# Kernel optimization log

Hardware: AMD Instinct MI355X
Metric: run time of the kernel (lower is better)

Reference implementation:

```python
import jax, jax.numpy as jnp
import numpy as np

B, S, N = 16, 128, 64            # batch, sentence length, padded KB-word slots per sentence
E, DK, H, L = 128, 128, 128, 32  # char embed, kb embed, per-direction hidden (hidden_size=2H), labels
CHAR_NUM, KB_NUM = 8000, 200000


def setup_inputs():
    key = jax.random.key(0)
    ks = jax.random.split(key, 40)
    u = lambda k, sh: jax.random.uniform(k, sh, jnp.float32, -0.08, 0.08)
    inp = {
        "char_ids": jax.random.randint(ks[0], (B, S), 0, CHAR_NUM),
        "kb_word_ids": jax.random.randint(ks[1], (B, N), 0, KB_NUM),
        "word_begin": jax.random.randint(ks[2], (B, N), 0, S),
        "word_len": jax.random.randint(ks[3], (B, N), 0, 6),
        "label": jax.random.randint(ks[4], (B, S), 0, L),
        "sequence_length": jax.random.randint(ks[5], (B,), S // 2, S + 1),
        "char_emb": u(ks[6], (CHAR_NUM, E)),
        "kb_emb": u(ks[7], (KB_NUM, DK)),
        "dense_W": u(ks[8], (2 * H, L)),
        "dense_b": jnp.zeros((L,), jnp.float32),
        "crf_T": u(ks[9], (L, L)),
    }
    i = 10
    for p in ("f", "r"):
        inp[p + "_Wcx"] = u(ks[i], (E, 4 * H))
        inp[p + "_Wch"] = u(ks[i + 1], (H, 4 * H))
        inp[p + "_bc"] = jnp.zeros((4 * H,), jnp.float32)
        inp[p + "_Wwx"] = u(ks[i + 2], (DK, 3 * H))
        inp[p + "_Wwh"] = u(ks[i + 3], (H, 3 * H))
        inp[p + "_bw"] = jnp.zeros((3 * H,), jnp.float32)
        inp[p + "_Wlx"] = u(ks[i + 4], (E, H))
        inp[p + "_Wlc"] = u(ks[i + 5], (H, H))
        inp[p + "_bl"] = jnp.zeros((H,), jnp.float32)
        i += 6
    return inp


def _lattice_dir(X, Xw, begin, end, pos_valid, word_valid,
                 Wcx, Wch, bc, Wwx, Wwh, bw, Wlx, Wlc, bl):
    # X:[S,E] chars in scan order, Xw:[N,DK] KB words, begin/end:[N] span indices
    # in scan order (end inclusive), pos_valid:[S] bool, word_valid:[N] bool.
    Xg = X @ Wcx + bc    # [S,4H] hoisted char-gate input projection
    Xl = X @ Wlx + bl    # [S,H]  hoisted link-gate input projection
    Wg = Xw @ Wwx + bw   # [N,3H] hoisted word-gate input projection

    def step(carry, t):
        h_hist, c_hist = carry                 # [S+1,H]; slot k = state after step k-1
        h_prev, c_prev = h_hist[t], c_hist[t]
        gi, gf, go, gg = jnp.split(Xg[t] + h_prev @ Wch, 4)
        i = jax.nn.sigmoid(gi); f = jax.nn.sigmoid(gf)
        o = jax.nn.sigmoid(go); g = jnp.tanh(gg)
        # word cells: built from the state just before each word's begin position
        hb, cb = h_hist[begin], c_hist[begin]  # [N,H]
        wi, wf, wg = jnp.split(Wg + hb @ Wwh, 3, axis=1)
        cw = jax.nn.sigmoid(wf) * cb + jax.nn.sigmoid(wi) * jnp.tanh(wg)  # [N,H]
        lg = jax.nn.sigmoid(Xl[t] + cw @ Wlc)  # [N,H] link gates
        wmask = ((end == t) & word_valid).astype(X.dtype)[:, None]
        ew = jnp.exp(lg) * wmask
        ec = jnp.exp(i)
        c_lat = (ec * g + (ew * cw).sum(0)) / (ec + ew.sum(0))  # gate-normalized merge
        c_std = f * c_prev + i * g             # plain LSTM step when no word ends at t
        c_t = jnp.where(wmask.sum() > 0, c_lat, c_std)
        h_t = o * jnp.tanh(c_t)
        v = pos_valid[t]
        h_hist = h_hist.at[t + 1].set(jnp.where(v, h_t, h_prev))
        c_hist = c_hist.at[t + 1].set(jnp.where(v, c_t, c_prev))
        return (h_hist, c_hist), jnp.where(v, h_t, jnp.zeros_like(h_t))

    init = (jnp.zeros((S + 1, H), X.dtype), jnp.zeros((S + 1, H), X.dtype))
    _, hs = jax.lax.scan(step, init, jnp.arange(S))
    return hs  # [S,H]


def _forward(char_ids, kb_word_ids, word_begin, word_len, label, sequence_length,
             char_emb, kb_emb, dense_W, dense_b, crf_T, fparams, rparams):
    X = char_emb[char_ids]            # [B,S,E]
    Xw = kb_emb[kb_word_ids]          # [B,N,DK]
    end = jnp.minimum(word_begin + word_len, S - 1)   # inclusive span end
    word_valid = end < sequence_length[:, None]       # whole span inside sentence
    pos = jnp.arange(S)
    pv_f = pos[None, :] < sequence_length[:, None]
    fwd = jax.vmap(lambda x, xw, b, e, pv, wv:
                   _lattice_dir(x, xw, b, e, pv, wv, *fparams))(
        X, Xw, word_begin, end, pv_f, word_valid)
    # backward direction: flip time axis; span (b,e) maps to (S-1-e, S-1-b)
    pv_r = pos[None, :] >= (S - sequence_length)[:, None]
    bwd = jax.vmap(lambda x, xw, b, e, pv, wv:
                   _lattice_dir(x, xw, b, e, pv, wv, *rparams))(
        X[:, ::-1], Xw, S - 1 - end, S - 1 - word_begin, pv_r, word_valid)[:, ::-1]
    feats = jnp.concatenate([fwd, bwd], axis=-1)      # [B,S,2H]
    logits = feats @ dense_W + dense_b                # [B,S,L]
    # CRF negative log-likelihood
    mask = pv_f.astype(logits.dtype)                  # [B,S]
    emit = jnp.take_along_axis(logits, label[..., None], axis=2)[..., 0]
    trans = crf_T[label[:, :-1], label[:, 1:]]
    gold = (emit * mask).sum(1) + (trans * mask[:, 1:]).sum(1)

    def fstep(alpha, xs):
        logit_t, m_t = xs
        new = jax.scipy.special.logsumexp(alpha[:, :, None] + crf_T[None], axis=1) + logit_t
        return jnp.where(m_t[:, None] > 0, new, alpha), None

    alpha, _ = jax.lax.scan(fstep, logits[:, 0],
                            (logits[:, 1:].transpose(1, 0, 2), mask[:, 1:].T))
    logZ = jax.scipy.special.logsumexp(alpha, axis=1)
    return jnp.mean(logZ - gold)


def reference(char_ids, kb_word_ids, word_begin, word_len, label, sequence_length,
              char_emb, kb_emb, dense_W, dense_b, crf_T,
              f_Wcx, f_Wch, f_bc, f_Wwx, f_Wwh, f_bw, f_Wlx, f_Wlc, f_bl,
              r_Wcx, r_Wch, r_bc, r_Wwx, r_Wwh, r_bw, r_Wlx, r_Wlc, r_bl):
    fparams = (f_Wcx, f_Wch, f_bc, f_Wwx, f_Wwh, f_bw, f_Wlx, f_Wlc, f_bl)
    rparams = (r_Wcx, r_Wch, r_bc, r_Wwx, r_Wwh, r_bw, r_Wlx, r_Wlc, r_bl)
    return _forward(char_ids, kb_word_ids, word_begin, word_len, label, sequence_length,
                    char_emb, kb_emb, dense_W, dense_b, crf_T, fparams, rparams)
```

## Files before the change

kernel.cpp:

```cpp
#include <hip/hip_runtime.h>


typedef _Float16 f16x8 __attribute__((ext_vector_type(8)));
typedef float    f32x4 __attribute__((ext_vector_type(4)));

__device__ __forceinline__ float sigm(float x) { return 1.f / (1.f + __expf(-x)); }
__device__ __forceinline__ float tanh_fast(float x) {
    return 1.f - 2.f / (__expf(2.f * x) + 1.f);
}
__device__ __forceinline__ void bar_lgkm() {
    asm volatile("s_waitcnt lgkmcnt(0)\n\ts_barrier" ::: "memory");
}

__device__ __forceinline__ f32x4 mfma16(f16x8 a, f16x8 b, f32x4 c) {
    return __builtin_amdgcn_mfma_f32_16x16x32_f16(a, b, c, 0, 0, 0);
}

__global__ __launch_bounds__(256)
void gemm_char(const float* __restrict__ emb, const int* __restrict__ idx,
               const float* __restrict__ Wg0, const float* __restrict__ Wg1,
               const float* __restrict__ bg0, const float* __restrict__ bg1,
               const float* __restrict__ Wl0, const float* __restrict__ Wl1,
               const float* __restrict__ bl0, const float* __restrict__ bl1,
               float* __restrict__ outg, float* __restrict__ outl)
{
    constexpr int K = 128, RPB = 8, BLK = 256;
    const int y = blockIdx.y;
    const float* __restrict__ Wg = y ? Wg1 : Wg0;
    const float* __restrict__ bg = y ? bg1 : bg0;
    const float* __restrict__ Wl = y ? Wl1 : Wl0;
    const float* __restrict__ bl = y ? bl1 : bl0;
    float* __restrict__ og = outg + (size_t)y * 2048 * 512;
    float* __restrict__ ol = outl + (size_t)y * 2048 * 128;

    __shared__ __align__(16) float xs[RPB * K];
    __shared__ const float* srcs[RPB];
    const int tid = threadIdx.x;
    const int r0 = blockIdx.x * RPB;
    if (tid < RPB) {
        const int row = r0 + tid;
        const int bb = row >> 7, tt = row & 127;
        const int ts = y ? (127 - tt) : tt;
        srcs[tid] = emb + (size_t)idx[bb * 128 + ts] * K;
    }
    __syncthreads();
    constexpr int NQ = RPB * K / 4;
    for (int q = tid; q < NQ; q += BLK) {
        const int rr = q / (K / 4), qq = q - rr * (K / 4);
        ((float4*)xs)[q] = ((const float4*)srcs[rr])[qq];
    }
    __syncthreads();

    {
        constexpr int NJ4 = 128, RT = BLK / NJ4, RPT = RPB / RT;
        const int jq = tid % NJ4;
        const int rg = tid / NJ4;
        float4 acc[RPT];
#pragma unroll
        for (int r = 0; r < RPT; ++r) acc[r] = make_float4(0.f, 0.f, 0.f, 0.f);
        const float4* __restrict__ W4 = (const float4*)Wg;
#pragma unroll 4
        for (int k = 0; k < K; ++k) {
            const float4 wv = W4[(size_t)k * NJ4 + jq];
#pragma unroll
            for (int r = 0; r < RPT; ++r) {
                const float xv = xs[(rg * RPT + r) * K + k];
                acc[r].x = fmaf(xv, wv.x, acc[r].x);
                acc[r].y = fmaf(xv, wv.y, acc[r].y);
                acc[r].z = fmaf(xv, wv.z, acc[r].z);
                acc[r].w = fmaf(xv, wv.w, acc[r].w);
            }
        }
        const float4 bv = ((const float4*)bg)[jq];
#pragma unroll
        for (int r = 0; r < RPT; ++r) {
            const int row = r0 + rg * RPT + r;
            ((float4*)og)[(size_t)row * NJ4 + jq] =
                make_float4(acc[r].x + bv.x, acc[r].y + bv.y,
                            acc[r].z + bv.z, acc[r].w + bv.w);
        }
    }
    {
        constexpr int NJ4 = 32;
        const int jq = tid % NJ4;
        const int rg = tid / NJ4;
        float4 acc = make_float4(0.f, 0.f, 0.f, 0.f);
        const float4* __restrict__ W4 = (const float4*)Wl;
#pragma unroll 4
        for (int k = 0; k < K; ++k) {
            const float4 wv = W4[(size_t)k * NJ4 + jq];
            const float xv = xs[rg * K + k];
            acc.x = fmaf(xv, wv.x, acc.x);
            acc.y = fmaf(xv, wv.y, acc.y);
            acc.z = fmaf(xv, wv.z, acc.z);
            acc.w = fmaf(xv, wv.w, acc.w);
        }
        const float4 bv = ((const float4*)bl)[jq];
        const int row = r0 + rg;
        ((float4*)ol)[(size_t)row * NJ4 + jq] =
            make_float4(acc.x + bv.x, acc.y + bv.y, acc.z + bv.z, acc.w + bv.w);
    }
}

template <int K, int J, int RPB, int BLK>
__global__ __launch_bounds__(BLK)
void gemm_pair(const float* __restrict__ emb, const int* __restrict__ idx,
               const float* __restrict__ W0, const float* __restrict__ W1,
               const float* __restrict__ b0, const float* __restrict__ b1,
               float* __restrict__ out, int rowsTotal, int Sdim, int revmode)
{
    constexpr int NJ4 = J / 4;
    constexpr int RT  = BLK / NJ4;
    constexpr int RPT = RPB / RT;
    static_assert(BLK % NJ4 == 0 && RPB % RT == 0, "layout");
    const int y = blockIdx.y;
    const float* __restrict__ W    = y ? W1 : W0;
    const float* __restrict__ bias = y ? b1 : b0;
    float* __restrict__ outp = out + (size_t)y * rowsTotal * J;
    const int rev = (revmode && y) ? 1 : 0;

    __shared__ __align__(16) float xs[RPB * K];
    __shared__ const float* srcs[RPB];
    const int tid = threadIdx.x;
    const int r0 = blockIdx.x * RPB;
    if (tid < RPB) {
        const int row = r0 + tid;
        const float* s = nullptr;
        if (row < rowsTotal) {
            if (idx) {
                const int bb = row / Sdim, tt = row - bb * Sdim;
                const int ts = rev ? (Sdim - 1 - tt) : tt;
                s = emb + (size_t)idx[bb * Sdim + ts] * K;
            } else {
                s = emb + (size_t)row * K;
            }
        }
        srcs[tid] = s;
    }
    __syncthreads();
    constexpr int NQ = RPB * K / 4;
    for (int q = tid; q < NQ; q += BLK) {
        const int rr = q / (K / 4), qq = q - rr * (K / 4);
        const float4* s = (const float4*)srcs[rr];
        ((float4*)xs)[q] = s ? s[qq] : make_float4(0.f, 0.f, 0.f, 0.f);
    }
    __syncthreads();

    const int jq = tid % NJ4;
    const int rg = tid / NJ4;
    float4 acc[RPT];
#pragma unroll
    for (int r = 0; r < RPT; ++r) acc[r] = make_float4(0.f, 0.f, 0.f, 0.f);
    const float4* __restrict__ W4 = (const float4*)W;
#pragma unroll 4
    for (int k = 0; k < K; ++k) {
        const float4 wv = W4[(size_t)k * NJ4 + jq];
#pragma unroll
        for (int r = 0; r < RPT; ++r) {
            const float xv = xs[(rg * RPT + r) * K + k];
            acc[r].x = fmaf(xv, wv.x, acc[r].x);
            acc[r].y = fmaf(xv, wv.y, acc[r].y);
            acc[r].z = fmaf(xv, wv.z, acc[r].z);
            acc[r].w = fmaf(xv, wv.w, acc[r].w);
        }
    }
    const float4 bv = ((const float4*)bias)[jq];
#pragma unroll
    for (int r = 0; r < RPT; ++r) {
        const int row = r0 + rg * RPT + r;
        if (row < rowsTotal)
            ((float4*)outp)[(size_t)row * NJ4 + jq] =
                make_float4(acc[r].x + bv.x, acc[r].y + bv.y,
                            acc[r].z + bv.z, acc[r].w + bv.w);
    }
}

#define HH_BYTES (129 * 128 * 2)
#define CH_BYTES (129 * 128 * 4)
#define LAT_DYN_SMEM (HH_BYTES + CH_BYTES)

__global__ __launch_bounds__(512, 2)
void lattice_kernel(const float* __restrict__ Xg,
                    const float* __restrict__ Xl,
                    const float* __restrict__ Wgp,
                    const float* __restrict__ Wch_f, const float* __restrict__ Wch_r,
                    const float* __restrict__ Wwh_f, const float* __restrict__ Wwh_r,
                    const float* __restrict__ Wlc_f, const float* __restrict__ Wlc_r,
                    const int* __restrict__ word_begin, const int* __restrict__ word_len,
                    const int* __restrict__ seqlen,
                    float* __restrict__ feats)
{
    extern __shared__ __align__(16) char dyn_smem[];
    _Float16* hh = (_Float16*)dyn_smem;
    float*    ch = (float*)(dyn_smem + HH_BYTES);

    const int bdid = blockIdx.x;
    const int b = bdid >> 1, dir = bdid & 1;
    const int tid = threadIdx.x;
    const int wid = tid >> 6;
    const int ln  = tid & 63;
    const int lg  = ln >> 4;
    const int jm  = wid * 16 + (ln & 15);

    const float* Wch = dir ? Wch_r : Wch_f;
    const float* Wwh = dir ? Wwh_r : Wwh_f;
    const float* Wlc = dir ? Wlc_r : Wlc_f;

    f16x8 Bc[4][4];
#pragma unroll
    for (int g = 0; g < 4; ++g)
#pragma unroll
        for (int kt = 0; kt < 4; ++kt) {
            f16x8 v;
#pragma unroll
            for (int i = 0; i < 8; ++i)
                v[i] = (_Float16)Wch[(size_t)(kt * 32 + lg * 8 + i) * 512 + (g * 128 + jm)];
            Bc[g][kt] = v;
        }
    f16x8 Bw[3][4];
#pragma unroll
    for (int p = 0; p < 3; ++p)
#pragma unroll
        for (int kt = 0; kt < 4; ++kt) {
            f16x8 v;
#pragma unroll
            for (int i = 0; i < 8; ++i)
                v[i] = (_Float16)Wwh[(size_t)(kt * 32 + lg * 8 + i) * 384 + (p * 128 + jm)];
            Bw[p][kt] = v;
        }
    f16x8 Bl[4];
#pragma unroll
    for (int kt = 0; kt < 4; ++kt) {
        f16x8 v;
#pragma unroll
        for (int i = 0; i < 8; ++i)
            v[i] = (_Float16)Wlc[(size_t)(kt * 32 + lg * 8 + i) * 128 + jm];
        Bl[kt] = v;
    }

    __shared__ __align__(16) _Float16 cw2s[2][2][128];
    __shared__ int ev_start[129];
    __shared__ int cnts[128];
    __shared__ int fills[128];
    __shared__ short ev_word[64];
    __shared__ short wbeg_s[64];

    const int sl = seqlen[b];

    if (tid < 128) { cnts[tid] = 0; fills[tid] = 0; }
    __syncthreads();
    int myvalid = 0, myed = 0;
    if (tid < 64) {
        const int bg = word_begin[b * 64 + tid];
        const int lnw = word_len[b * 64 + tid];
        int ef = bg + lnw; if (ef > 127) ef = 127;
        myvalid = (ef < sl);
        const int bd_ = dir ? (127 - ef) : bg;
        const int ed_ = dir ? (127 - bg) : ef;
        wbeg_s[tid] = (short)bd_;
        myed = ed_;
        if (myvalid) atomicAdd(&cnts[ed_], 1);
    }
    __syncthreads();
    if (tid == 0) {
        int run = 0; ev_start[0] = 0;
        for (int t = 0; t < 128; ++t) { run += cnts[t]; ev_start[t + 1] = run; }
    }
    __syncthreads();
    if (tid < 64 && myvalid) {
        const int pos = atomicAdd(&fills[myed], 1);
        ev_word[ev_start[myed] + pos] = (short)tid;
    }
    if (tid < 128) { hh[tid] = (_Float16)0.f; ch[tid] = 0.f; }
    __syncthreads();

    const float* Xg_b = Xg + ((size_t)dir * 2048 + (size_t)b * 128) * 512;
    const float* Xl_b = Xl + ((size_t)dir * 2048 + (size_t)b * 128) * 128;
    const float* Wg_b = Wgp + ((size_t)dir * 1024 + (size_t)b * 64) * 384;

    float h_reg = 0.f, c_reg = 0.f;

    int   curE, cur_ec0;
    int   cur_bgs[2] = {0, 0};
    float cur_wgp[2][3] = {};
    float xg_cur[4];
    {
        curE = ev_start[1];
        cur_ec0 = curE < 2 ? curE : 2;
#pragma unroll
        for (int s = 0; s < 2; ++s)
            if (s < cur_ec0) {
                const int wd = __builtin_amdgcn_readfirstlane((int)ev_word[s]);
                cur_bgs[s] = __builtin_amdgcn_readfirstlane((int)wbeg_s[wd]);
                const float* wgr = Wg_b + (size_t)wd * 384;
                cur_wgp[s][0] = wgr[jm];
                cur_wgp[s][1] = wgr[128 + jm];
                cur_wgp[s][2] = wgr[256 + jm];
            }
#pragma unroll
        for (int g = 0; g < 4; ++g) xg_cur[g] = Xg_b[g * 128 + jm];
    }

    for (int t = 0; t < 128; ++t) {
        f16x8 A[4];
#pragma unroll
        for (int kt = 0; kt < 4; ++kt)
            A[kt] = ((const f16x8*)hh)[t * 16 + kt * 4 + lg];

        float xl = 0.f;
        if (curE > 0) xl = Xl_b[(size_t)t * 128 + jm];

        int   nxtE = 0, nxt_ec0 = 0;
        int   nxt_bgs[2] = {0, 0};
        float nxt_wgp[2][3] = {};
        float xg_nxt[4] = {0.f, 0.f, 0.f, 0.f};
        if (t < 127) {
            const int e0n = ev_start[t + 1];
            nxtE = ev_start[t + 2] - e0n;
            nxt_ec0 = nxtE < 2 ? nxtE : 2;
#pragma unroll
            for (int s = 0; s < 2; ++s)
                if (s < nxt_ec0) {
                    const int wd = __builtin_amdgcn_readfirstlane((int)ev_word[e0n + s]);
                    nxt_bgs[s] = __builtin_amdgcn_readfirstlane((int)wbeg_s[wd]);
                    const float* wgr = Wg_b + (size_t)wd * 384;
                    nxt_wgp[s][0] = wgr[jm];
                    nxt_wgp[s][1] = wgr[128 + jm];
                    nxt_wgp[s][2] = wgr[256 + jm];
                }
#pragma unroll
            for (int g = 0; g < 4; ++g)
                xg_nxt[g] = Xg_b[(size_t)(t + 1) * 512 + g * 128 + jm];
        }

        f32x4 d[4];
#pragma unroll
        for (int g = 0; g < 4; ++g) d[g] = (f32x4){0.f, 0.f, 0.f, 0.f};
#pragma unroll
        for (int kt = 0; kt < 4; ++kt)
#pragma unroll
            for (int g = 0; g < 4; ++g)
                d[g] = mfma16(A[kt], Bc[g][kt], d[g]);

        const float gi = sigm(d[0][0] + xg_cur[0]);
        const float gf = sigm(d[1][0] + xg_cur[1]);
        const float go = sigm(d[2][0] + xg_cur[2]);
        const float gg = tanh_fast(d[3][0] + xg_cur[3]);

        float accn = 0.f, accd = 0.f;
        if (curE > 0) {
            const int e0 = ev_start[t];
            float cwreg[2] = {0.f, 0.f};
#pragma unroll
            for (int s = 0; s < 2; ++s)
                if (s < cur_ec0) {
                    f16x8 Ab[4];
#pragma unroll
                    for (int kt = 0; kt < 4; ++kt)
                        Ab[kt] = ((const f16x8*)hh)[cur_bgs[s] * 16 + kt * 4 + lg];
                    f32x4 ep[3];
#pragma unroll
                    for (int p = 0; p < 3; ++p) ep[p] = (f32x4){0.f, 0.f, 0.f, 0.f};
#pragma unroll
                    for (int kt = 0; kt < 4; ++kt)
#pragma unroll
                        for (int p = 0; p < 3; ++p)
                            ep[p] = mfma16(Ab[kt], Bw[p][kt], ep[p]);
                    const float wi = cur_wgp[s][0] + ep[0][0];
                    const float wf = cur_wgp[s][1] + ep[1][0];
                    const float wv = cur_wgp[s][2] + ep[2][0];
                    const float cb = ch[(size_t)cur_bgs[s] * 128 + jm];
                    const float cwv = sigm(wf) * cb + sigm(wi) * tanh_fast(wv);
                    cwreg[s] = cwv;
                    if (ln < 16) cw2s[0][s][jm] = (_Float16)cwv;
                }
            bar_lgkm();
#pragma unroll
            for (int s = 0; s < 2; ++s)
                if (s < cur_ec0) {
                    f16x8 Ac[4];
#pragma unroll
                    for (int kt = 0; kt < 4; ++kt)
                        Ac[kt] = ((const f16x8*)(&cw2s[0][s][0]))[kt * 4 + lg];
                    f32x4 r = (f32x4){0.f, 0.f, 0.f, 0.f};
#pragma unroll
                    for (int kt = 0; kt < 4; ++kt)
                        r = mfma16(Ac[kt], Bl[kt], r);
                    const float lgv = sigm(xl + r[0]);
                    const float ew = __expf(lgv);
                    accn = fmaf(ew, cwreg[s], accn);
                    accd += ew;
                }
            for (int base2 = 2; base2 < curE; base2 += 2) {
                const int bb = (base2 >> 1) & 1;
                const int en = (curE - base2) < 2 ? (curE - base2) : 2;
                float cwr2[2] = {0.f, 0.f};
#pragma unroll
                for (int s = 0; s < 2; ++s)
                    if (s < en) {
                        const int wd = __builtin_amdgcn_readfirstlane((int)ev_word[e0 + base2 + s]);
                        const int bg2 = __builtin_amdgcn_readfirstlane((int)wbeg_s[wd]);
                        const float* wgr = Wg_b + (size_t)wd * 384;
                        const float wg0 = wgr[jm], wg1 = wgr[128 + jm], wg2 = wgr[256 + jm];
                        f16x8 Ab[4];
#pragma unroll
                        for (int kt = 0; kt < 4; ++kt)
                            Ab[kt] = ((const f16x8*)hh)[bg2 * 16 + kt * 4 + lg];
                        f32x4 ep[3];
#pragma unroll
                        for (int p = 0; p < 3; ++p) ep[p] = (f32x4){0.f, 0.f, 0.f, 0.f};
#pragma unroll
                        for (int kt = 0; kt < 4; ++kt)
#pragma unroll
                            for (int p = 0; p < 3; ++p)
                                ep[p] = mfma16(Ab[kt], Bw[p][kt], ep[p]);
                        const float wi = wg0 + ep[0][0];
                        const float wf = wg1 + ep[1][0];
                        const float wv = wg2 + ep[2][0];
                        const float cb = ch[(size_t)bg2 * 128 + jm];
                        const float cwv = sigm(wf) * cb + sigm(wi) * tanh_fast(wv);
                        cwr2[s] = cwv;
                        if (ln < 16) cw2s[bb][s][jm] = (_Float16)cwv;
                    }
                bar_lgkm();
#pragma unroll
                for (int s = 0; s < 2; ++s)
                    if (s < en) {
                        f16x8 Ac[4];
#pragma unroll
                        for (int kt = 0; kt < 4; ++kt)
                            Ac[kt] = ((const f16x8*)(&cw2s[bb][s][0]))[kt * 4 + lg];
                        f32x4 r = (f32x4){0.f, 0.f, 0.f, 0.f};
#pragma unroll
                        for (int kt = 0; kt < 4; ++kt)
                            r = mfma16(Ac[kt], Bl[kt], r);
                        const float lgv = sigm(xl + r[0]);
                        const float ew = __expf(lgv);
                        accn = fmaf(ew, cwr2[s], accn);
                        accd += ew;
                    }
            }
        }

        float c_t;
        if (curE > 0) {
            const float ec = __expf(gi);
            c_t = (ec * gg + accn) / (ec + accd);
        } else {
            c_t = gf * c_reg + gi * gg;
        }
        const float h_t = go * tanh_fast(c_t);
        const bool v = dir ? (t >= 128 - sl) : (t < sl);
        const float hn = v ? h_t : h_reg;
        const float cn = v ? c_t : c_reg;
        h_reg = hn; c_reg = cn;
        if (ln < 16) {
            hh[(size_t)(t + 1) * 128 + jm] = (_Float16)hn;
            ch[(size_t)(t + 1) * 128 + jm] = cn;
        }

        curE = nxtE; cur_ec0 = nxt_ec0;
        cur_bgs[0] = nxt_bgs[0]; cur_bgs[1] = nxt_bgs[1];
#pragma unroll
        for (int s = 0; s < 2; ++s) {
            cur_wgp[s][0] = nxt_wgp[s][0];
            cur_wgp[s][1] = nxt_wgp[s][1];
            cur_wgp[s][2] = nxt_wgp[s][2];
        }
#pragma unroll
        for (int g = 0; g < 4; ++g) xg_cur[g] = xg_nxt[g];
        bar_lgkm();
    }

    for (int i = tid; i < 128 * 128; i += 512) {
        const int t = i >> 7, j = i & 127;
        const bool v = dir ? (t >= 128 - sl) : (t < sl);
        const float hv = v ? (float)hh[(size_t)(t + 1) * 128 + j] : 0.f;
        const int s = dir ? (127 - t) : t;
        feats[((size_t)b * 128 + s) * 256 + dir * 128 + j] = hv;
    }
}

__global__ void crf_kernel(const float* __restrict__ logits,
                           const int* __restrict__ label,
                           const int* __restrict__ seqlen,
                           const float* __restrict__ T,
                           float* __restrict__ out_part)
{
    const int half = threadIdx.x >> 5;
    const int j    = threadIdx.x & 31;
    const int b    = blockIdx.x * 2 + half;

    float Tc[32];
#pragma unroll
    for (int i = 0; i < 32; ++i) Tc[i] = T[i * 32 + j];

    const float* lg = logits + (size_t)b * 128 * 32;
    const int* lab = label + b * 128;
    const int sl = seqlen[b];

    float g = 0.f;
#pragma unroll
    for (int r = 0; r < 4; ++r) {
        const int t = j + r * 32;
        if (t < sl) {
            g += lg[t * 32 + lab[t]];
            if (t >= 1) g += T[lab[t - 1] * 32 + lab[t]];
        }
    }
#pragma unroll
    for (int m = 16; m; m >>= 1) g += __shfl_xor(g, m, 32);

    __shared__ __align__(16) float alpha_s[2][32];
    float av = lg[j];
    alpha_s[half][j] = av;
    __syncthreads();
    for (int t = 1; t < 128; ++t) {
        float a[32];
        const float4* ap = (const float4*)alpha_s[half];
#pragma unroll
        for (int q = 0; q < 8; ++q) {
            const float4 v = ap[q];
            a[4 * q] = v.x; a[4 * q + 1] = v.y; a[4 * q + 2] = v.z; a[4 * q + 3] = v.w;
        }
        float m = -1e30f;
#pragma unroll
        for (int i = 0; i < 32; ++i) m = fmaxf(m, a[i] + Tc[i]);
        float s = 0.f;
#pragma unroll
        for (int i = 0; i < 32; ++i) s += __expf(a[i] + Tc[i] - m);
        float nv = m + __logf(s) + lg[t * 32 + j];
        if (t >= sl) nv = av;
        av = nv;
        __syncthreads();
        alpha_s[half][j] = av;
        __syncthreads();
    }
    float m2 = av;
#pragma unroll
    for (int m = 16; m; m >>= 1) m2 = fmaxf(m2, __shfl_xor(m2, m, 32));
    float s2 = __expf(av - m2);
#pragma unroll
    for (int m = 16; m; m >>= 1) s2 += __shfl_xor(s2, m, 32);
    if (j == 0) out_part[b] = (m2 + __logf(s2)) - g;
}

__global__ void finalize_kernel(const float* __restrict__ partb, float* __restrict__ out)
{
    if (threadIdx.x == 0 && blockIdx.x == 0) {
        float s = 0.f;
        for (int i = 0; i < 16; i++) s += partb[i];
        out[0] = s * (1.f / 16.f);
    }
}

extern "C" void kernel_launch(void* const* d_in, const int* in_sizes, int n_in,
                              void* d_out, int out_size, void* d_ws, size_t ws_size,
                              hipStream_t stream)
{
    (void)in_sizes; (void)n_in; (void)out_size; (void)ws_size;
    const int*   char_ids    = (const int*)d_in[0];
    const int*   kb_word_ids = (const int*)d_in[1];
    const int*   word_begin  = (const int*)d_in[2];
    const int*   word_len    = (const int*)d_in[3];
    const int*   label       = (const int*)d_in[4];
    const int*   seqlen      = (const int*)d_in[5];
    const float* char_emb    = (const float*)d_in[6];
    const float* kb_emb      = (const float*)d_in[7];
    const float* dense_W     = (const float*)d_in[8];
    const float* dense_b     = (const float*)d_in[9];
    const float* crf_T       = (const float*)d_in[10];
    const float* f_Wcx = (const float*)d_in[11];
    const float* f_Wch = (const float*)d_in[12];
    const float* f_bc  = (const float*)d_in[13];
    const float* f_Wwx = (const float*)d_in[14];
    const float* f_Wwh = (const float*)d_in[15];
    const float* f_bw  = (const float*)d_in[16];
    const float* f_Wlx = (const float*)d_in[17];
    const float* f_Wlc = (const float*)d_in[18];
    const float* f_bl  = (const float*)d_in[19];
    const float* r_Wcx = (const float*)d_in[20];
    const float* r_Wch = (const float*)d_in[21];
    const float* r_bc  = (const float*)d_in[22];
    const float* r_Wwx = (const float*)d_in[23];
    const float* r_Wwh = (const float*)d_in[24];
    const float* r_bw  = (const float*)d_in[25];
    const float* r_Wlx = (const float*)d_in[26];
    const float* r_Wlc = (const float*)d_in[27];
    const float* r_bl  = (const float*)d_in[28];

    float* ws = (float*)d_ws;
    size_t o = 0;
    float* Xg     = ws + o; o += (size_t)2 * 2048 * 512;
    float* Xl     = ws + o; o += (size_t)2 * 2048 * 128;
    float* Wg     = ws + o; o += (size_t)2 * 1024 * 384;
    float* feats  = ws + o; o += (size_t)2048 * 256;
    float* logits = ws + o; o += (size_t)2048 * 32;
    float* partb  = ws + o; o += 16;

    gemm_char<<<dim3(256, 2), 256, 0, stream>>>(
        char_emb, char_ids, f_Wcx, r_Wcx, f_bc, r_bc,
        f_Wlx, r_Wlx, f_bl, r_bl, Xg, Xl);
    gemm_pair<128, 384, 8, 192><<<dim3(128, 2), 192, 0, stream>>>(
        kb_emb, kb_word_ids, f_Wwx, r_Wwx, f_bw, r_bw, Wg, 1024, 64, 0);

    lattice_kernel<<<32, 512, LAT_DYN_SMEM, stream>>>(
        Xg, Xl, Wg, f_Wch, r_Wch, f_Wwh, r_Wwh, f_Wlc, r_Wlc,
        word_begin, word_len, seqlen, feats);

    gemm_pair<256, 32, 16, 128><<<dim3(128, 1), 128, 0, stream>>>(
        feats, nullptr, dense_W, dense_W, dense_b, dense_b, logits, 2048, 128, 0);
    crf_kernel<<<8, 64, 0, stream>>>(logits, label, seqlen, crf_T, partb);
    finalize_kernel<<<1, 64, 0, stream>>>(partb, (float*)d_out);
}
```

Measured before the change: 496.4 us.

## Fuse pre-GEMMs, dense projection into lattice, and finalize into CRF

Merges the char and KB-word input projections into a single launch, computes per-direction partial logits inside the lattice kernel with fp16 dot2 instead of writing feats and running a separate dense GEMM, and folds the final mean into the CRF kernel using an atomic completion counter. The goal is to cut three kernel launches and the round trip of the feats buffer through global memory. In exchange the dense projection now runs in fp16, which changes numerics, and correctness depends on the counter being reset by the pre-GEMM kernel on every call.

```diff
diff --git a/kernel.cpp b/kernel.cpp
--- a/kernel.cpp
+++ b/kernel.cpp
@@ -1,6 +1,7 @@
 #include <hip/hip_runtime.h>
 
 
+typedef _Float16 f16x2 __attribute__((ext_vector_type(2)));
 typedef _Float16 f16x8 __attribute__((ext_vector_type(8)));
 typedef float    f32x4 __attribute__((ext_vector_type(4)));
 
@@ -16,162 +17,158 @@
     return __builtin_amdgcn_mfma_f32_16x16x32_f16(a, b, c, 0, 0, 0);
 }
 
+#if defined(__has_builtin)
+#if __has_builtin(__builtin_amdgcn_fdot2)
+#define FDOT2(a, b, c) __builtin_amdgcn_fdot2((a), (b), (c), false)
+#endif
+#endif
+#ifndef FDOT2
+__device__ __forceinline__ float fdot2_sw(f16x2 a, f16x2 b, float c) {
+    return fmaf((float)a.x, (float)b.x, fmaf((float)a.y, (float)b.y, c));
+}
+#define FDOT2(a, b, c) fdot2_sw((a), (b), (c))
+#endif
+
 __global__ __launch_bounds__(256)
-void gemm_char(const float* __restrict__ emb, const int* __restrict__ idx,
-               const float* __restrict__ Wg0, const float* __restrict__ Wg1,
-               const float* __restrict__ bg0, const float* __restrict__ bg1,
-               const float* __restrict__ Wl0, const float* __restrict__ Wl1,
-               const float* __restrict__ bl0, const float* __restrict__ bl1,
-               float* __restrict__ outg, float* __restrict__ outl)
+void gemm_pre(const float* __restrict__ cemb, const int* __restrict__ cidx,
+              const float* __restrict__ kemb, const int* __restrict__ kidx,
+              const float* __restrict__ Wg0, const float* __restrict__ Wg1,
+              const float* __restrict__ bg0, const float* __restrict__ bg1,
+              const float* __restrict__ Wl0, const float* __restrict__ Wl1,
+              const float* __restrict__ bl0, const float* __restrict__ bl1,
+              const float* __restrict__ Ww0, const float* __restrict__ Ww1,
+              const float* __restrict__ bw0, const float* __restrict__ bw1,
+              float* __restrict__ outg, float* __restrict__ outl,
+              float* __restrict__ outw, int* __restrict__ done_cnt)
 {
     constexpr int K = 128, RPB = 8, BLK = 256;
     const int y = blockIdx.y;
-    const float* __restrict__ Wg = y ? Wg1 : Wg0;
-    const float* __restrict__ bg = y ? bg1 : bg0;
-    const float* __restrict__ Wl = y ? Wl1 : Wl0;
-    const float* __restrict__ bl = y ? bl1 : bl0;
-    float* __restrict__ og = outg + (size_t)y * 2048 * 512;
-    float* __restrict__ ol = outl + (size_t)y * 2048 * 128;
+    const int tid = threadIdx.x;
+    if (blockIdx.x == 0 && y == 0 && tid == 0) *done_cnt = 0;
 
     __shared__ __align__(16) float xs[RPB * K];
     __shared__ const float* srcs[RPB];
-    const int tid = threadIdx.x;
-    const int r0 = blockIdx.x * RPB;
-    if (tid < RPB) {
-        const int row = r0 + tid;
-        const int bb = row >> 7, tt = row & 127;
-        const int ts = y ? (127 - tt) : tt;
-        srcs[tid] = emb + (size_t)idx[bb * 128 + ts] * K;
-    }
-    __syncthreads();
-    constexpr int NQ = RPB * K / 4;
-    for (int q = tid; q < NQ; q += BLK) {
-        const int rr = q / (K / 4), qq = q - rr * (K / 4);
-        ((float4*)xs)[q] = ((const float4*)srcs[rr])[qq];
-    }
-    __syncthreads();
-
-    {
-        constexpr int NJ4 = 128, RT = BLK / NJ4, RPT = RPB / RT;
-        const int jq = tid % NJ4;
-        const int rg = tid / NJ4;
-        float4 acc[RPT];
-#pragma unroll
-        for (int r = 0; r < RPT; ++r) acc[r] = make_float4(0.f, 0.f, 0.f, 0.f);
-        const float4* __restrict__ W4 = (const float4*)Wg;
+
+    if (blockIdx.x < 256) {
+        const float* __restrict__ Wg = y ? Wg1 : Wg0;
+        const float* __restrict__ bg = y ? bg1 : bg0;
+        const float* __restrict__ Wl = y ? Wl1 : Wl0;
+        const float* __restrict__ bl = y ? bl1 : bl0;
+        float* __restrict__ og = outg + (size_t)y * 2048 * 512;
+        float* __restrict__ ol = outl + (size_t)y * 2048 * 128;
+
+        const int r0 = blockIdx.x * RPB;
+        if (tid < RPB) {
+            const int row = r0 + tid;
+            const int bb = row >> 7, tt = row & 127;
+            const int ts = y ? (127 - tt) : tt;
+            srcs[tid] = cemb + (size_t)cidx[bb * 128 + ts] * K;
+        }
+        __syncthreads();
+        constexpr int NQ = RPB * K / 4;
+        for (int q = tid; q < NQ; q += BLK) {
+            const int rr = q / (K / 4), qq = q - rr * (K / 4);
+            ((float4*)xs)[q] = ((const float4*)srcs[rr])[qq];
+        }
+        __syncthreads();
+
+        {
+            constexpr int NJ4 = 128, RT = BLK / NJ4, RPT = RPB / RT;
+            const int jq = tid % NJ4;
+            const int rg = tid / NJ4;
+            float4 acc[RPT];
+#pragma unroll
+            for (int r = 0; r < RPT; ++r) acc[r] = make_float4(0.f, 0.f, 0.f, 0.f);
+            const float4* __restrict__ W4 = (const float4*)Wg;
 #pragma unroll 4
-        for (int k = 0; k < K; ++k) {
-            const float4 wv = W4[(size_t)k * NJ4 + jq];
+            for (int k = 0; k < K; ++k) {
+                const float4 wv = W4[(size_t)k * NJ4 + jq];
+#pragma unroll
+                for (int r = 0; r < RPT; ++r) {
+                    const float xv = xs[(rg * RPT + r) * K + k];
+                    acc[r].x = fmaf(xv, wv.x, acc[r].x);
+                    acc[r].y = fmaf(xv, wv.y, acc[r].y);
+                    acc[r].z = fmaf(xv, wv.z, acc[r].z);
+                    acc[r].w = fmaf(xv, wv.w, acc[r].w);
+                }
+            }
+            const float4 bv = ((const float4*)bg)[jq];
 #pragma unroll
             for (int r = 0; r < RPT; ++r) {
-                const float xv = xs[(rg * RPT + r) * K + k];
-                acc[r].x = fmaf(xv, wv.x, acc[r].x);
-                acc[r].y = fmaf(xv, wv.y, acc[r].y);
-                acc[r].z = fmaf(xv, wv.z, acc[r].z);
-                acc[r].w = fmaf(xv, wv.w, acc[r].w);
-            }
-        }
-        const float4 bv = ((const float4*)bg)[jq];
-#pragma unroll
-        for (int r = 0; r < RPT; ++r) {
-            const int row = r0 + rg * RPT + r;
-            ((float4*)og)[(size_t)row * NJ4 + jq] =
-                make_float4(acc[r].x + bv.x, acc[r].y + bv.y,
-                            acc[r].z + bv.z, acc[r].w + bv.w);
-        }
-    }
-    {
-        constexpr int NJ4 = 32;
-        const int jq = tid % NJ4;
-        const int rg = tid / NJ4;
-        float4 acc = make_float4(0.f, 0.f, 0.f, 0.f);
-        const float4* __restrict__ W4 = (const float4*)Wl;
+                const int row = r0 + rg * RPT + r;
+                ((float4*)og)[(size_t)row * NJ4 + jq] =
+                    make_float4(acc[r].x + bv.x, acc[r].y + bv.y,
+                                acc[r].z + bv.z, acc[r].w + bv.w);
+            }
+        }
+        {
+            constexpr int NJ4 = 32;
+            const int jq = tid % NJ4;
+            const int rg = tid / NJ4;
+            float4 acc = make_float4(0.f, 0.f, 0.f, 0.f);
+            const float4* __restrict__ W4 = (const float4*)Wl;
 #pragma unroll 4
-        for (int k = 0; k < K; ++k) {
-            const float4 wv = W4[(size_t)k * NJ4 + jq];
-            const float xv = xs[rg * K + k];
-            acc.x = fmaf(xv, wv.x, acc.x);
-            acc.y = fmaf(xv, wv.y, acc.y);
-            acc.z = fmaf(xv, wv.z, acc.z);
-            acc.w = fmaf(xv, wv.w, acc.w);
-        }
-        const float4 bv = ((const float4*)bl)[jq];
-        const int row = r0 + rg;
-        ((float4*)ol)[(size_t)row * NJ4 + jq] =
-            make_float4(acc.x + bv.x, acc.y + bv.y, acc.z + bv.z, acc.w + bv.w);
-    }
-}
-
-template <int K, int J, int RPB, int BLK>
-__global__ __launch_bounds__(BLK)
-void gemm_pair(const float* __restrict__ emb, const int* __restrict__ idx,
-               const float* __restrict__ W0, const float* __restrict__ W1,
-               const float* __restrict__ b0, const float* __restrict__ b1,
-               float* __restrict__ out, int rowsTotal, int Sdim, int revmode)
-{
-    constexpr int NJ4 = J / 4;
-    constexpr int RT  = BLK / NJ4;
-    constexpr int RPT = RPB / RT;
-    static_assert(BLK % NJ4 == 0 && RPB % RT == 0, "layout");
-    const int y = blockIdx.y;
-    const float* __restrict__ W    = y ? W1 : W0;
-    const float* __restrict__ bias = y ? b1 : b0;
-    float* __restrict__ outp = out + (size_t)y * rowsTotal * J;
-    const int rev = (revmode && y) ? 1 : 0;
-
-    __shared__ __align__(16) float xs[RPB * K];
-    __shared__ const float* srcs[RPB];
-    const int tid = threadIdx.x;
-    const int r0 = blockIdx.x * RPB;
-    if (tid < RPB) {
-        const int row = r0 + tid;
-        const float* s = nullptr;
-        if (row < rowsTotal) {
-            if (idx) {
-                const int bb = row / Sdim, tt = row - bb * Sdim;
-                const int ts = rev ? (Sdim - 1 - tt) : tt;
-                s = emb + (size_t)idx[bb * Sdim + ts] * K;
-            } else {
-                s = emb + (size_t)row * K;
-            }
-        }
-        srcs[tid] = s;
-    }
-    __syncthreads();
-    constexpr int NQ = RPB * K / 4;
-    for (int q = tid; q < NQ; q += BLK) {
-        const int rr = q / (K / 4), qq = q - rr * (K / 4);
-        const float4* s = (const float4*)srcs[rr];
-        ((float4*)xs)[q] = s ? s[qq] : make_float4(0.f, 0.f, 0.f, 0.f);
-    }
-    __syncthreads();
-
-    const int jq = tid % NJ4;
-    const int rg = tid / NJ4;
-    float4 acc[RPT];
-#pragma unroll
-    for (int r = 0; r < RPT; ++r) acc[r] = make_float4(0.f, 0.f, 0.f, 0.f);
-    const float4* __restrict__ W4 = (const float4*)W;
+            for (int k = 0; k < K; ++k) {
+                const float4 wv = W4[(size_t)k * NJ4 + jq];
+                const float xv = xs[rg * K + k];
+                acc.x = fmaf(xv, wv.x, acc.x);
+                acc.y = fmaf(xv, wv.y, acc.y);
+                acc.z = fmaf(xv, wv.z, acc.z);
+                acc.w = fmaf(xv, wv.w, acc.w);
+            }
+            const float4 bv = ((const float4*)bl)[jq];
+            const int row = r0 + rg;
+            ((float4*)ol)[(size_t)row * NJ4 + jq] =
+                make_float4(acc.x + bv.x, acc.y + bv.y, acc.z + bv.z, acc.w + bv.w);
+        }
+    } else {
+        const float* __restrict__ Ww = y ? Ww1 : Ww0;
+        const float* __restrict__ bw = y ? bw1 : bw0;
+        float* __restrict__ ow = outw + (size_t)y * 1024 * 384;
+
+        const int r0 = (blockIdx.x - 256) * RPB;
+        if (tid < RPB) {
+            const int row = r0 + tid;
+            const int bb = row >> 6, tt = row & 63;
+            srcs[tid] = kemb + (size_t)kidx[bb * 64 + tt] * K;
+        }
+        __syncthreads();
+        constexpr int NQ = RPB * K / 4;
+        for (int q = tid; q < NQ; q += BLK) {
+            const int rr = q / (K / 4), qq = q - rr * (K / 4);
+            ((float4*)xs)[q] = ((const float4*)srcs[rr])[qq];
+        }
+        __syncthreads();
+
+        constexpr int NJ4 = 96, RPT = 4;
+        if (tid < 192) {
+            const int jq = tid % NJ4;
+            const int rg = tid / NJ4;
+            float4 acc[RPT];
+#pragma unroll
+            for (int r = 0; r < RPT; ++r) acc[r] = make_float4(0.f, 0.f, 0.f, 0.f);
+            const float4* __restrict__ W4 = (const float4*)Ww;
 #pragma unroll 4
-    for (int k = 0; k < K; ++k) {
-        const float4 wv = W4[(size_t)k * NJ4 + jq];
-#pragma unroll
-        for (int r = 0; r < RPT; ++r) {
-            const float xv = xs[(rg * RPT + r) * K + k];
-            acc[r].x = fmaf(xv, wv.x, acc[r].x);
-            acc[r].y = fmaf(xv, wv.y, acc[r].y);
-            acc[r].z = fmaf(xv, wv.z, acc[r].z);
-            acc[r].w = fmaf(xv, wv.w, acc[r].w);
-        }
-    }
-    const float4 bv = ((const float4*)bias)[jq];
-#pragma unroll
-    for (int r = 0; r < RPT; ++r) {
-        const int row = r0 + rg * RPT + r;
-        if (row < rowsTotal)
-            ((float4*)outp)[(size_t)row * NJ4 + jq] =
-                make_float4(acc[r].x + bv.x, acc[r].y + bv.y,
-                            acc[r].z + bv.z, acc[r].w + bv.w);
+            for (int k = 0; k < K; ++k) {
+                const float4 wv = W4[(size_t)k * NJ4 + jq];
+#pragma unroll
+                for (int r = 0; r < RPT; ++r) {
+                    const float xv = xs[(rg * RPT + r) * K + k];
+                    acc[r].x = fmaf(xv, wv.x, acc[r].x);
+                    acc[r].y = fmaf(xv, wv.y, acc[r].y);
+                    acc[r].z = fmaf(xv, wv.z, acc[r].z);
+                    acc[r].w = fmaf(xv, wv.w, acc[r].w);
+                }
+            }
+            const float4 bv = ((const float4*)bw)[jq];
+#pragma unroll
+            for (int r = 0; r < RPT; ++r) {
+                const int row = r0 + rg * RPT + r;
+                ((float4*)ow)[(size_t)row * NJ4 + jq] =
+                    make_float4(acc[r].x + bv.x, acc[r].y + bv.y,
+                                acc[r].z + bv.z, acc[r].w + bv.w);
+            }
+        }
     }
 }
 
@@ -186,9 +183,10 @@
                     const float* __restrict__ Wch_f, const float* __restrict__ Wch_r,
                     const float* __restrict__ Wwh_f, const float* __restrict__ Wwh_r,
                     const float* __restrict__ Wlc_f, const float* __restrict__ Wlc_r,
+                    const float* __restrict__ dense_W, const float* __restrict__ dense_b,
                     const int* __restrict__ word_begin, const int* __restrict__ word_len,
                     const int* __restrict__ seqlen,
-                    float* __restrict__ feats)
+                    float* __restrict__ plog)
 {
     extern __shared__ __align__(16) char dyn_smem[];
     _Float16* hh = (_Float16*)dyn_smem;
@@ -472,20 +470,42 @@
         bar_lgkm();
     }
 
-    for (int i = tid; i < 128 * 128; i += 512) {
-        const int t = i >> 7, j = i & 127;
-        const bool v = dir ? (t >= 128 - sl) : (t < sl);
-        const float hv = v ? (float)hh[(size_t)(t + 1) * 128 + j] : 0.f;
-        const int s = dir ? (127 - t) : t;
-        feats[((size_t)b * 128 + s) * 256 + dir * 128 + j] = hv;
-    }
-}
-
-__global__ void crf_kernel(const float* __restrict__ logits,
+    {
+        f16x2* Wd2 = (f16x2*)ch;
+        for (int i = tid; i < 64 * 32; i += 512) {
+            const int kk = i >> 5, j = i & 31;
+            f16x2 v;
+            v.x = (_Float16)dense_W[(size_t)(dir * 128 + 2 * kk) * 32 + j];
+            v.y = (_Float16)dense_W[(size_t)(dir * 128 + 2 * kk + 1) * 32 + j];
+            Wd2[i] = v;
+        }
+        bar_lgkm();
+        const int j  = tid & 31;
+        const int t0 = tid >> 5;
+        const float bj = dir ? 0.f : dense_b[j];
+        for (int p = 0; p < 8; ++p) {
+            const int t = p * 16 + t0;
+            const bool v = dir ? (t >= 128 - sl) : (t < sl);
+            float acc = bj;
+            if (v) {
+                const f16x2* hrow = (const f16x2*)(hh + (size_t)(t + 1) * 128);
+#pragma unroll
+                for (int kk = 0; kk < 64; ++kk)
+                    acc = FDOT2(Wd2[kk * 32 + j], hrow[kk], acc);
+            }
+            const int s = dir ? (127 - t) : t;
+            plog[((size_t)dir * 2048 + (size_t)b * 128 + s) * 32 + j] = acc;
+        }
+    }
+}
+
+__global__ void crf_kernel(const float* __restrict__ plog,
                            const int* __restrict__ label,
                            const int* __restrict__ seqlen,
                            const float* __restrict__ T,
-                           float* __restrict__ out_part)
+                           float* __restrict__ out_part,
+                           int* __restrict__ done_cnt,
+                           float* __restrict__ out)
 {
     const int half = threadIdx.x >> 5;
     const int j    = threadIdx.x & 31;
@@ -495,7 +515,8 @@
 #pragma unroll
     for (int i = 0; i < 32; ++i) Tc[i] = T[i * 32 + j];
 
-    const float* lg = logits + (size_t)b * 128 * 32;
+    const float* lgA = plog + (size_t)b * 128 * 32;
+    const float* lgB = plog + (size_t)2048 * 32 + (size_t)b * 128 * 32;
     const int* lab = label + b * 128;
     const int sl = seqlen[b];
 
@@ -504,7 +525,7 @@
     for (int r = 0; r < 4; ++r) {
         const int t = j + r * 32;
         if (t < sl) {
-            g += lg[t * 32 + lab[t]];
+            g += lgA[t * 32 + lab[t]] + lgB[t * 32 + lab[t]];
             if (t >= 1) g += T[lab[t - 1] * 32 + lab[t]];
         }
     }
@@ -512,7 +533,7 @@
     for (int m = 16; m; m >>= 1) g += __shfl_xor(g, m, 32);
 
     __shared__ __align__(16) float alpha_s[2][32];
-    float av = lg[j];
+    float av = lgA[j] + lgB[j];
     alpha_s[half][j] = av;
     __syncthreads();
     for (int t = 1; t < 128; ++t) {
@@ -529,7 +550,7 @@
         float s = 0.f;
 #pragma unroll
         for (int i = 0; i < 32; ++i) s += __expf(a[i] + Tc[i] - m);
-        float nv = m + __logf(s) + lg[t * 32 + j];
+        float nv = m + __logf(s) + (lgA[t * 32 + j] + lgB[t * 32 + j]);
         if (t >= sl) nv = av;
         av = nv;
         __syncthreads();
@@ -543,14 +564,17 @@
 #pragma unroll
     for (int m = 16; m; m >>= 1) s2 += __shfl_xor(s2, m, 32);
     if (j == 0) out_part[b] = (m2 + __logf(s2)) - g;
-}
-
-__global__ void finalize_kernel(const float* __restrict__ partb, float* __restrict__ out)
-{
-    if (threadIdx.x == 0 && blockIdx.x == 0) {
-        float s = 0.f;
-        for (int i = 0; i < 16; i++) s += partb[i];
-        out[0] = s * (1.f / 16.f);
+
+    __syncthreads();
+    if (threadIdx.x == 0) {
+        __threadfence();
+        const int old = atomicAdd(done_cnt, 1);
+        if (old == 7) {
+            __threadfence();
+            float s = 0.f;
+            for (int i = 0; i < 16; ++i) s += out_part[i];
+            out[0] = s * (1.f / 16.f);
+        }
     }
 }
 
@@ -594,22 +618,21 @@
     float* Xg     = ws + o; o += (size_t)2 * 2048 * 512;
     float* Xl     = ws + o; o += (size_t)2 * 2048 * 128;
     float* Wg     = ws + o; o += (size_t)2 * 1024 * 384;
-    float* feats  = ws + o; o += (size_t)2048 * 256;
-    float* logits = ws + o; o += (size_t)2048 * 32;
+    float* plog   = ws + o; o += (size_t)2 * 2048 * 32;
     float* partb  = ws + o; o += 16;
-
-    gemm_char<<<dim3(256, 2), 256, 0, stream>>>(
-        char_emb, char_ids, f_Wcx, r_Wcx, f_bc, r_bc,
-        f_Wlx, r_Wlx, f_bl, r_bl, Xg, Xl);
-    gemm_pair<128, 384, 8, 192><<<dim3(128, 2), 192, 0, stream>>>(
-        kb_emb, kb_word_ids, f_Wwx, r_Wwx, f_bw, r_bw, Wg, 1024, 64, 0);
+    int*   dcnt   = (int*)(ws + o); o += 1;
+
+    gemm_pre<<<dim3(384, 2), 256, 0, stream>>>(
+        char_emb, char_ids, kb_emb, kb_word_ids,
+        f_Wcx, r_Wcx, f_bc, r_bc,
+        f_Wlx, r_Wlx, f_bl, r_bl,
+        f_Wwx, r_Wwx, f_bw, r_bw,
+        Xg, Xl, Wg, dcnt);
 
     lattice_kernel<<<32, 512, LAT_DYN_SMEM, stream>>>(
         Xg, Xl, Wg, f_Wch, r_Wch, f_Wwh, r_Wwh, f_Wlc, r_Wlc,
-        word_begin, word_len, seqlen, feats);
-
-    gemm_pair<256, 32, 16, 128><<<dim3(128, 1), 128, 0, stream>>>(
-        feats, nullptr, dense_W, dense_W, dense_b, dense_b, logits, 2048, 128, 0);
-    crf_kernel<<<8, 64, 0, stream>>>(logits, label, seqlen, crf_T, partb);
-    finalize_kernel<<<1, 64, 0, stream>>>(partb, (float*)d_out);
-}
+        dense_W, dense_b, word_begin, word_len, seqlen, plog);
+
+    crf_kernel<<<8, 64, 0, stream>>>(plog, label, seqlen, crf_T,
+                                     partb, dcnt, (float*)d_out);
+}
```

New measurement: 463.8 us (median of 2 runs). 6.6% less time.
